# Kernel optimization log

Measured on AMD Instinct MI355X. Metric: run time of the kernel, lower is better.

## Reference

```python
import jax, jax.numpy as jnp
import numpy as np

DIM = 256
CTX_DIM = 256
HEADS = 32
DIM_HEAD = 32
INNER = HEADS * DIM_HEAD


def mish(x):
    return x * jnp.tanh(jax.nn.softplus(x))


def setup_inputs() -> dict:
    key = jax.random.key(0)
    ks = jax.random.split(key, 16)
    B, Lq, Lp = 16, 128, 512
    s = 0.02
    return {
        "x": jax.random.normal(ks[0], (B * Lq, DIM), jnp.float32),
        "context": jax.random.normal(ks[1], (B * Lp, CTX_DIM), jnp.float32),
        "batch_dis": jax.random.normal(ks[2], (B, Lp, Lq, 3), jnp.float32),
        "batch_dis_emb": jax.random.normal(ks[3], (B, Lp, Lq, HEADS), jnp.float32),
        "protein_len": Lp,
        "ligand_len": Lq,
        # params ([in, out] layout, torch Linear transposed)
        "W_qk": jax.random.normal(ks[4], (DIM, INNER), jnp.float32) * s,
        "W_v": jax.random.normal(ks[5], (DIM, INNER), jnp.float32) * s,
        "W_cqk": jax.random.normal(ks[6], (CTX_DIM, INNER), jnp.float32) * s,
        "W_cv": jax.random.normal(ks[7], (CTX_DIM, INNER), jnp.float32) * s,
        "W_m1": jax.random.normal(ks[8], (2 * HEADS, 4 * HEADS), jnp.float32) * s,
        "W_m2": jax.random.normal(ks[9], (4 * HEADS, 2 * HEADS), jnp.float32) * s,
        "b_m2": jnp.zeros((2 * HEADS,), jnp.float32),
        "W_o": jax.random.normal(ks[10], (INNER, DIM), jnp.float32) * s,
        "b_o": jnp.zeros((DIM,), jnp.float32),
        "W_d1": jax.random.normal(ks[11], (HEADS, 2 * HEADS), jnp.float32) * s,
        "b_d1": jnp.zeros((2 * HEADS,), jnp.float32),
        "W_d2": jax.random.normal(ks[12], (2 * HEADS, HEADS), jnp.float32) * s,
        "b_d2": jnp.zeros((HEADS,), jnp.float32),
    }


def reference(x, context, batch_dis, batch_dis_emb, protein_len, ligand_len,
              W_qk, W_v, W_cqk, W_cv, W_m1, W_m2, b_m2, W_o, b_o,
              W_d1, b_d1, W_d2, b_d2):
    h, dh = HEADS, DIM_HEAD
    scale = dh ** -0.5
    B = x.shape[0] // ligand_len
    # projections; split heads: [B, L, h, dh]
    qk = (x @ W_qk).reshape(B, ligand_len, h, dh)
    cqk = (context @ W_cqk).reshape(B, protein_len, h, dh)
    cv = (context @ W_cv).reshape(B, protein_len, h, dh)
    # ligand->protein attention scores: [B, h, Lq, Lp]
    sim = jnp.einsum('bihd,bjhd->bhij', qk, cqk) * scale
    # distance-embedding channels: [B, Lp, Lq, h] -> [B, h, Lq, Lp]
    dis = jnp.transpose(batch_dis_emb, (0, 3, 2, 1))
    s = jnp.concatenate([sim, dis], axis=1)           # [B, 2h, Lq, Lp]
    s = jnp.moveaxis(s, 1, -1)                        # [B, Lq, Lp, 2h]
    s = mish(s @ W_m1) @ W_m2 + b_m2                  # attn_mlp over channel dim
    attn = jax.nn.softmax(s, axis=2)                  # softmax over protein (j)
    # first h heads attend into context values
    out = jnp.einsum('bijh,bjhd->bihd', attn[..., :h], cv)
    out = out.reshape(B * ligand_len, h * dh) @ W_o + b_o   # [N_lig, dim]
    # last h heads aggregate 3D distance vectors
    out_dis = jnp.einsum('bijh,bjid->bidh', attn[..., h:], batch_dis)
    out_dis = out_dis.reshape(B * ligand_len, 3, h)
    out_dis = mish(out_dis @ W_d1 + b_d1) @ W_d2 + b_d2      # [N_lig, 3, h]
    return out, out_dis
```

## Files before the change

kernel.cpp:

```cpp
#include <hip/hip_runtime.h>

typedef unsigned short u16;
typedef unsigned int   u32;
typedef __attribute__((ext_vector_type(8))) short bf16x8;
typedef __attribute__((ext_vector_type(4))) float f32x4;

#define MFMA_BF16 __builtin_amdgcn_mfma_f32_16x16x32_bf16
#define LOG2E 1.4426950408889634f

__device__ __forceinline__ u16 f2bf(float f) {
    u32 x = __builtin_bit_cast(u32, f);
    u32 r = (x + 0x7fffu + ((x >> 16) & 1u)) >> 16;
    return (u16)r;
}
__device__ __forceinline__ u32 cvt_pk_bf16(float lo, float hi) {
    u32 r;
    asm("v_cvt_pk_bf16_f32 %0, %1, %2" : "=v"(r) : "v"(lo), "v"(hi));
    return r;
}
__device__ __forceinline__ float exp2_asm(float x) {
    float r;
    asm("v_exp_f32 %0, %1" : "=v"(r) : "v"(x));
    return r;
}
__device__ __forceinline__ float rcp_asm(float x) {
    float r;
    asm("v_rcp_f32 %0, %1" : "=v"(r) : "v"(x));
    return r;
}
__device__ __forceinline__ float mishf(float x) {
    float e = exp2_asm(x * LOG2E);
    float p = 1.f + e;
    float d = __builtin_fmaf(p, p, 1.f);
    float r = __builtin_fmaf(-2.f, rcp_asm(d), 1.f);
    return x * r;
}

__global__ __launch_bounds__(256) void gemm_mfma(
    const float* __restrict__ A, const float* __restrict__ W, u16* __restrict__ C,
    int M, int N, int K, float scale)
{
    __shared__ u16 As[128 * 40];
    __shared__ u16 Bf[8 * 64 * 8];

    const int tid = threadIdx.x;
    const int lane = tid & 63, wv = tid >> 6;
    const int qd = lane >> 4, ln = lane & 15;
    const int m0 = blockIdx.y * 128, n0 = blockIdx.x * 128;

    f32x4 acc[2][8];
#pragma unroll
    for (int a = 0; a < 2; ++a)
#pragma unroll
        for (int nt = 0; nt < 8; ++nt) acc[a][nt] = (f32x4){0.f, 0.f, 0.f, 0.f};

    for (int k0 = 0; k0 < K; k0 += 32) {
        {
            int r = tid >> 1, kh = (tid & 1) * 16;
            const float* ap = A + (size_t)(m0 + r) * K + k0 + kh;
            float4 a0 = ((const float4*)ap)[0];
            float4 a1 = ((const float4*)ap)[1];
            float4 a2 = ((const float4*)ap)[2];
            float4 a3 = ((const float4*)ap)[3];
            uint4 p0, p1;
            p0.x = cvt_pk_bf16(a0.x, a0.y);
            p0.y = cvt_pk_bf16(a0.z, a0.w);
            p0.z = cvt_pk_bf16(a1.x, a1.y);
            p0.w = cvt_pk_bf16(a1.z, a1.w);
            p1.x = cvt_pk_bf16(a2.x, a2.y);
            p1.y = cvt_pk_bf16(a2.z, a2.w);
            p1.z = cvt_pk_bf16(a3.x, a3.y);
            p1.w = cvt_pk_bf16(a3.z, a3.w);
            *(uint4*)&As[r * 40 + kh]     = p0;
            *(uint4*)&As[r * 40 + kh + 8] = p1;
        }
        {
            int ntA = tid >> 6, q = (tid >> 4) & 3, nn = tid & 15;
#pragma unroll
            for (int h = 0; h < 2; ++h) {
                int nt = ntA + h * 4;
                const float* wp = W + (size_t)(k0 + q * 8) * N + n0 + nt * 16 + nn;
                float w0 = wp[0], w1 = wp[(size_t)1 * N], w2 = wp[(size_t)2 * N], w3 = wp[(size_t)3 * N];
                float w4 = wp[(size_t)4 * N], w5 = wp[(size_t)5 * N], w6 = wp[(size_t)6 * N], w7 = wp[(size_t)7 * N];
                uint4 u;
                u.x = cvt_pk_bf16(w0, w1);
                u.y = cvt_pk_bf16(w2, w3);
                u.z = cvt_pk_bf16(w4, w5);
                u.w = cvt_pk_bf16(w6, w7);
                *(uint4*)&Bf[(nt * 64 + q * 16 + nn) * 8] = u;
            }
        }
        __syncthreads();
        bf16x8 af0 = *(const bf16x8*)&As[(wv * 32 + ln) * 40 + qd * 8];
        bf16x8 af1 = *(const bf16x8*)&As[(wv * 32 + 16 + ln) * 40 + qd * 8];
#pragma unroll
        for (int nt = 0; nt < 8; ++nt) {
            bf16x8 bfr = *(const bf16x8*)&Bf[(nt * 64 + lane) * 8];
            acc[0][nt] = MFMA_BF16(af0, bfr, acc[0][nt], 0, 0, 0);
            acc[1][nt] = MFMA_BF16(af1, bfr, acc[1][nt], 0, 0, 0);
        }
        __syncthreads();
    }
#pragma unroll
    for (int a = 0; a < 2; ++a)
#pragma unroll
        for (int nt = 0; nt < 8; ++nt) {
            u32 pk0 = cvt_pk_bf16(acc[a][nt][0] * scale, acc[a][nt][1] * scale);
            u32 pk1 = cvt_pk_bf16(acc[a][nt][2] * scale, acc[a][nt][3] * scale);
            size_t base = (size_t)(m0 + wv * 32 + a * 16 + qd * 4) * N + n0 + nt * 16 + ln;
            C[base]               = (u16)pk0;
            C[base + (size_t)N]   = (u16)(pk0 >> 16);
            C[base + (size_t)2*N] = (u16)pk1;
            C[base + (size_t)3*N] = (u16)(pk1 >> 16);
        }
}

__global__ __launch_bounds__(256) void transpose_cv(
    const u16* __restrict__ cv, u16* __restrict__ cvT)
{
    __shared__ u16 T[64 * 80];
    const int tid = threadIdx.x;
    const int ct = blockIdx.x * 64, jt = blockIdx.y * 64, b = blockIdx.z;
    {
        int j_l = tid >> 2, seg = tid & 3;
        const u16* src = cv + (size_t)(b * 512 + jt + j_l) * 1024 + ct + seg * 16;
        uint4 v0 = ((const uint4*)src)[0];
        uint4 v1 = ((const uint4*)src)[1];
        u16* tp = &T[seg * 16 * 80 + j_l];
        tp[0*80] = (u16)(v0.x & 0xffff); tp[1*80] = (u16)(v0.x >> 16);
        tp[2*80] = (u16)(v0.y & 0xffff); tp[3*80] = (u16)(v0.y >> 16);
        tp[4*80] = (u16)(v0.z & 0xffff); tp[5*80] = (u16)(v0.z >> 16);
        tp[6*80] = (u16)(v0.w & 0xffff); tp[7*80] = (u16)(v0.w >> 16);
        tp[8*80] = (u16)(v1.x & 0xffff); tp[9*80] = (u16)(v1.x >> 16);
        tp[10*80] = (u16)(v1.y & 0xffff); tp[11*80] = (u16)(v1.y >> 16);
        tp[12*80] = (u16)(v1.z & 0xffff); tp[13*80] = (u16)(v1.z >> 16);
        tp[14*80] = (u16)(v1.w & 0xffff); tp[15*80] = (u16)(v1.w >> 16);
    }
    __syncthreads();
    {
        int ch_l = tid >> 2, sg = tid & 3;
        u16* dst = cvT + (size_t)(b * 1024 + ct + ch_l) * 512 + jt + sg * 16;
        ((uint4*)dst)[0] = *(const uint4*)&T[ch_l * 80 + sg * 16];
        ((uint4*)dst)[1] = *(const uint4*)&T[ch_l * 80 + sg * 16 + 8];
    }
}

__global__ __launch_bounds__(256) void prep(
    const float* __restrict__ Wo, const float* __restrict__ W1, const float* __restrict__ W2,
    u16* __restrict__ WoT, u16* __restrict__ w1b, u16* __restrict__ w2b)
{
    const int bb = blockIdx.x, t = threadIdx.x;
    if (bb < 256) {
#pragma unroll
        for (int kk = 0; kk < 4; ++kk)
            WoT[(size_t)t * 1024 + bb * 4 + kk] = f2bf(Wo[(size_t)(bb * 4 + kk) * 256 + t]);
    } else {
        for (int u = 0; u < 32; ++u) {
            int idx = t + 256 * u;
            int j = idx & 7, lane = (idx >> 3) & 63, f = idx >> 9;
            int n = lane & 15, q = lane >> 4, ntc = f & 7, ks = f >> 3;
            w1b[idx] = f2bf(W1[(ks * 32 + q * 8 + j) * 128 + ntc * 16 + n]);
        }
        for (int u = 0; u < 32; ++u) {
            int idx = t + 256 * u;
            int j = idx & 7, lane = (idx >> 3) & 63, f = idx >> 9;
            int n = lane & 15, q = lane >> 4, ot = f & 3, ks = f >> 2;
            int k = q * 8 + j;
            int ch = ((k & 1) << 4) | (k >> 1);
            w2b[idx] = f2bf(W2[(ks * 32 + ch) * 64 + ot * 16 + n] * LOG2E);
        }
    }
}

__global__ __launch_bounds__(256, 1) void attn5(
    const u16* __restrict__ qk,
    const u16* __restrict__ cqk,
    const u16* __restrict__ cvT,
    const float* __restrict__ bde,
    const float* __restrict__ bdis,
    const u16* __restrict__ w1b, const u16* __restrict__ w2b,
    const float* __restrict__ b2,
    float* __restrict__ partial)
{
    __shared__ __align__(16) char smem[76288];
    u16*   ES  = (u16*)smem;
    u16*   MT  = (u16*)(smem + 20480);
    float* BD  = (float*)(smem + 30720);
    u16*   EST = (u16*)(smem + 34816);
    u16*   W1B = (u16*)(smem + 59904);

    const int tid = threadIdx.x;
    const int lane = tid & 63, wv = tid >> 6;
    const int qd = lane >> 4, ln = lane & 15;
    const int nblk = blockIdx.x;
    const int xcd = nblk & 7, g = nblk >> 3;
    const int b = xcd * 2 + (g & 1);
    const int r2 = g >> 1;
    const int it = r2 >> 2, jq = r2 & 3;
    const int i0 = it * 16;
    const int pidx = (b * 8 + it) * 4 + jq;

    for (int k = tid; k < 4096; k += 256) ((u32*)W1B)[k] = ((const u32*)w1b)[k];

    float b2r[4];
#pragma unroll
    for (int ot = 0; ot < 4; ++ot) b2r[ot] = b2[ot * 16 + ln] * LOG2E;

    bf16x8 qkf[8];
#pragma unroll
    for (int hh = 0; hh < 8; ++hh) {
        int h = wv * 8 + hh;
        qkf[hh] = *(const bf16x8*)(qk + ((size_t)(b * 128 + i0 + ln)) * 1024 + h * 32 + qd * 8);
    }

    const int ii = tid & 15, jj = tid >> 4;

    bf16x8 cqk_pf[8];
    float4 bde_pf[8];
    float bdp0, bdp1, bdp2;
    {
        const u16* crow = cqk + (size_t)(b * 512 + jq * 128 + ln) * 1024 + qd * 8;
#pragma unroll
        for (int hh = 0; hh < 8; ++hh)
            cqk_pf[hh] = *(const bf16x8*)(crow + (wv * 8 + hh) * 32);
#pragma unroll
        for (int s2 = 0; s2 < 4; ++s2) {
            const float* dps = bde + (((size_t)(b * 512 + jq * 128 + ln)) * 128 + i0 + wv * 4 + s2) * 32 + qd * 8;
            bde_pf[s2 * 2]     = ((const float4*)dps)[0];
            bde_pf[s2 * 2 + 1] = ((const float4*)dps)[1];
        }
        const float* sp = bdis + ((size_t)(b * 512 + jq * 128 + jj) * 128 + i0 + ii) * 3;
        bdp0 = sp[0]; bdp1 = sp[1]; bdp2 = sp[2];
        float* dp2 = &BD[(ii * 16 + jj) * 4];
        dp2[0] = bdp0; dp2[1] = bdp1; dp2[2] = bdp2;
    }

    f32x4 oacc[8][2];
#pragma unroll
    for (int a = 0; a < 8; ++a)
#pragma unroll
        for (int c = 0; c < 2; ++c) oacc[a][c] = (f32x4){0.f, 0.f, 0.f, 0.f};
    float dn[4][4] = {};
    float dd[4][3][2] = {};

    __syncthreads();

#pragma clang loop unroll(disable)
    for (int ps = 0; ps < 8; ++ps) {
        const int jg0 = jq * 128 + ps * 16;

        {
            bf16x8 cqk_use[8];
#pragma unroll
            for (int hh = 0; hh < 8; ++hh) cqk_use[hh] = cqk_pf[hh];
#pragma unroll
            for (int hh = 0; hh < 4; ++hh) {
                const int h0 = wv * 8 + hh * 2;
                f32x4 c0 = (f32x4){0.f, 0.f, 0.f, 0.f}, c1 = c0;
                c0 = MFMA_BF16(qkf[hh * 2],     cqk_use[hh * 2],     c0, 0, 0, 0);
                c1 = MFMA_BF16(qkf[hh * 2 + 1], cqk_use[hh * 2 + 1], c1, 0, 0, 0);
#pragma unroll
                for (int r = 0; r < 4; ++r)
                    *(u32*)&ES[((qd * 4 + r) * 16 + ln) * 40 + h0] = cvt_pk_bf16(c0[r], c1[r]);
            }
        }
        __syncthreads();

        const int psn = (ps < 7) ? ps + 1 : 7;
        const int jgn = jq * 128 + psn * 16;
        float4 bde_use[8];
#pragma unroll
        for (int k = 0; k < 8; ++k) bde_use[k] = bde_pf[k];
        {
            const u16* crow = cqk + (size_t)(b * 512 + jgn + ln) * 1024 + qd * 8;
#pragma unroll
            for (int hh = 0; hh < 8; ++hh)
                cqk_pf[hh] = *(const bf16x8*)(crow + (wv * 8 + hh) * 32);
#pragma unroll
            for (int s2 = 0; s2 < 4; ++s2) {
                const float* dps = bde + (((size_t)(b * 512 + jgn + ln)) * 128 + i0 + wv * 4 + s2) * 32 + qd * 8;
                bde_pf[s2 * 2]     = ((const float4*)dps)[0];
                bde_pf[s2 * 2 + 1] = ((const float4*)dps)[1];
            }
            const float* sp = bdis + ((size_t)(b * 512 + jgn + jj) * 128 + i0 + ii) * 3;
            bdp0 = sp[0]; bdp1 = sp[1]; bdp2 = sp[2];
        }

#pragma unroll
        for (int s = 0; s < 4; ++s) {
            const int i_loc = wv * 4 + s;
            bf16x8 af0 = *(const bf16x8*)&ES[(i_loc * 16 + ln) * 40 + qd * 8];
            bf16x8 af1;
            {
                float4 a0 = bde_use[s * 2];
                float4 a1 = bde_use[s * 2 + 1];
                uint4 u;
                u.x = cvt_pk_bf16(a0.x, a0.y);
                u.y = cvt_pk_bf16(a0.z, a0.w);
                u.z = cvt_pk_bf16(a1.x, a1.y);
                u.w = cvt_pk_bf16(a1.z, a1.w);
                af1 = __builtin_bit_cast(bf16x8, u);
            }
            f32x4 uacc[4];
#pragma unroll
            for (int ot = 0; ot < 4; ++ot) uacc[ot] = (f32x4){0.f, 0.f, 0.f, 0.f};
#pragma unroll
            for (int cg = 0; cg < 4; ++cg) {
                u16* mtp = MT + wv * 1280 + (cg & 1) * 640;
                bf16x8 w00 = *(const bf16x8*)&W1B[((cg * 2 + 0) * 64 + lane) * 8];
                bf16x8 w01 = *(const bf16x8*)&W1B[((cg * 2 + 1) * 64 + lane) * 8];
                bf16x8 w10 = *(const bf16x8*)&W1B[((8 + cg * 2 + 0) * 64 + lane) * 8];
                bf16x8 w11 = *(const bf16x8*)&W1B[((8 + cg * 2 + 1) * 64 + lane) * 8];
                f32x4 t0 = (f32x4){0.f, 0.f, 0.f, 0.f}, t1 = t0;
                t0 = MFMA_BF16(af0, w00, t0, 0, 0, 0);
                t0 = MFMA_BF16(af1, w10, t0, 0, 0, 0);
                t1 = MFMA_BF16(af0, w01, t1, 0, 0, 0);
                t1 = MFMA_BF16(af1, w11, t1, 0, 0, 0);
#pragma unroll
                for (int r = 0; r < 4; ++r) {
                    u32 pk = cvt_pk_bf16(mishf(t0[r]), mishf(t1[r]));
                    *(u32*)&mtp[(qd * 4 + r) * 40 + (ln << 1)] = pk;
                }
                bf16x8 ta = *(const bf16x8*)&mtp[ln * 40 + qd * 8];
#pragma unroll
                for (int ot = 0; ot < 4; ++ot) {
                    bf16x8 wf = *(const bf16x8*)(w2b + ((size_t)(cg * 4 + ot) * 64 + lane) * 8);
                    uacc[ot] = MFMA_BF16(ta, wf, uacc[ot], 0, 0, 0);
                }
            }
            float Ev[4][4];
#pragma unroll
            for (int ot = 0; ot < 4; ++ot) {
#pragma unroll
                for (int r = 0; r < 4; ++r) Ev[ot][r] = exp2_asm(uacc[ot][r] + b2r[ot]);
                dn[s][ot] += (Ev[ot][0] + Ev[ot][1]) + (Ev[ot][2] + Ev[ot][3]);
            }
#pragma unroll
            for (int r = 0; r < 4; ++r) {
                float4 bp = *(const float4*)&BD[(i_loc * 16 + qd * 4 + r) * 4];
                dd[s][0][0] += Ev[2][r] * bp.x; dd[s][0][1] += Ev[3][r] * bp.x;
                dd[s][1][0] += Ev[2][r] * bp.y; dd[s][1][1] += Ev[3][r] * bp.y;
                dd[s][2][0] += Ev[2][r] * bp.z; dd[s][2][1] += Ev[3][r] * bp.z;
            }
#pragma unroll
            for (int ot = 0; ot < 2; ++ot) {
                const int base = (ot * 16 + ln) * 392 + i_loc * 24 + qd * 4;
                *(u32*)&EST[base]     = cvt_pk_bf16(Ev[ot][0], Ev[ot][1]);
                *(u32*)&EST[base + 2] = cvt_pk_bf16(Ev[ot][2], Ev[ot][3]);
            }
        }
        __syncthreads();

        {
            float* dp2 = &BD[(ii * 16 + jj) * 4];
            dp2[0] = bdp0; dp2[1] = bdp1; dp2[2] = bdp2;
        }
#pragma unroll
        for (int hh = 0; hh < 8; ++hh) {
            const int h = wv * 8 + hh;
            bf16x8 af = (bf16x8){0, 0, 0, 0, 0, 0, 0, 0};
            if (qd < 2) af = *(const bf16x8*)&EST[h * 392 + ln * 24 + qd * 8];
#pragma unroll
            for (int nt = 0; nt < 2; ++nt) {
                bf16x8 bfr = (bf16x8){0, 0, 0, 0, 0, 0, 0, 0};
                if (qd < 2)
                    bfr = *(const bf16x8*)(cvT + ((size_t)(b * 1024 + h * 32 + nt * 16 + ln)) * 512 + jg0 + qd * 8);
                oacc[hh][nt] = MFMA_BF16(af, bfr, oacc[hh][nt], 0, 0, 0);
            }
        }
    }

    float* P = partial + (size_t)pidx * 18944;
#pragma unroll
    for (int hh = 0; hh < 8; ++hh)
#pragma unroll
        for (int nt = 0; nt < 2; ++nt)
#pragma unroll
            for (int r = 0; r < 4; ++r)
                P[(size_t)(qd * 4 + r) * 1024 + (wv * 8 + hh) * 32 + nt * 16 + ln] = oacc[hh][nt][r];
#pragma unroll
    for (int s = 0; s < 4; ++s)
#pragma unroll
        for (int ot = 0; ot < 4; ++ot) {
            float v = dn[s][ot];
            v += __shfl_xor(v, 16, 64);
            v += __shfl_xor(v, 32, 64);
            if (qd == 0) P[16384 + (wv * 4 + s) * 64 + ot * 16 + ln] = v;
        }
#pragma unroll
    for (int s = 0; s < 4; ++s)
#pragma unroll
        for (int d = 0; d < 3; ++d)
#pragma unroll
            for (int o = 0; o < 2; ++o) {
                float v = dd[s][d][o];
                v += __shfl_xor(v, 16, 64);
                v += __shfl_xor(v, 32, 64);
                if (qd == 0) P[17408 + (wv * 4 + s) * 96 + d * 32 + o * 16 + ln] = v;
            }
}

__global__ __launch_bounds__(256, 2) void finalize(
    const float* __restrict__ partial, const u16* __restrict__ WoT,
    const float* __restrict__ bo,
    const float* __restrict__ Wd1, const float* __restrict__ bd1,
    const float* __restrict__ Wd2, const float* __restrict__ bd2,
    float* __restrict__ out0, float* __restrict__ out1)
{
    __shared__ float denomL[1024];
    __shared__ u16 preL[16 * 1032];
    __shared__ float odisL[1536];
    __shared__ float r1L[3072];

    const int tid = threadIdx.x;
    const int f = blockIdx.x;
    const int b = f >> 3, it = f & 7;
    const int row0 = b * 128 + it * 16;
    const float* P0 = partial + (size_t)(f * 4 + 0) * 18944;
    const float* P1 = partial + (size_t)(f * 4 + 1) * 18944;
    const float* P2 = partial + (size_t)(f * 4 + 2) * 18944;
    const float* P3 = partial + (size_t)(f * 4 + 3) * 18944;

    for (int k = tid; k < 1024; k += 256)
        denomL[k] = P0[16384 + k] + P1[16384 + k] + P2[16384 + k] + P3[16384 + k];
    __syncthreads();

    {
        const int h = tid >> 3;
#pragma unroll
        for (int i = 0; i < 16; ++i) {
            float4 a = *(const float4*)&P0[(size_t)i * 1024 + tid * 4];
            float4 bq = *(const float4*)&P1[(size_t)i * 1024 + tid * 4];
            float4 c = *(const float4*)&P2[(size_t)i * 1024 + tid * 4];
            float4 d = *(const float4*)&P3[(size_t)i * 1024 + tid * 4];
            float rdn = 1.f / denomL[i * 64 + h];
            u32 p0 = cvt_pk_bf16((a.x + bq.x + c.x + d.x) * rdn, (a.y + bq.y + c.y + d.y) * rdn);
            u32 p1 = cvt_pk_bf16((a.z + bq.z + c.z + d.z) * rdn, (a.w + bq.w + c.w + d.w) * rdn);
            *(uint2*)(void*)&preL[i * 1032 + tid * 4] = make_uint2(p0, p1);
        }
    }
    for (int idx = tid; idx < 1536; idx += 256) {
        int i = idx / 96, rm = idx % 96, h = rm & 31;
        odisL[idx] = (P0[17408 + idx] + P1[17408 + idx] + P2[17408 + idx] + P3[17408 + idx])
                     / denomL[i * 64 + 32 + h];
    }
    __syncthreads();

    {
        const int lane = tid & 63, wv = tid >> 6;
        const int qd = lane >> 4, ln = lane & 15;
        f32x4 acc[4];
#pragma unroll
        for (int nt = 0; nt < 4; ++nt) acc[nt] = (f32x4){0.f, 0.f, 0.f, 0.f};
#pragma clang loop unroll(disable)
        for (int ks = 0; ks < 32; ++ks) {
            bf16x8 af = *(const bf16x8*)&preL[ln * 1032 + ks * 32 + qd * 8];
#pragma unroll
            for (int nt = 0; nt < 4; ++nt) {
                bf16x8 wf = *(const bf16x8*)(WoT + ((size_t)(wv * 64 + nt * 16 + ln)) * 1024 + ks * 32 + qd * 8);
                acc[nt] = MFMA_BF16(af, wf, acc[nt], 0, 0, 0);
            }
        }
#pragma unroll
        for (int nt = 0; nt < 4; ++nt) {
            int col = wv * 64 + nt * 16 + ln;
            float bv = bo[col];
#pragma unroll
            for (int r = 0; r < 4; ++r)
                out0[(size_t)(row0 + qd * 4 + r) * 256 + col] = acc[nt][r] + bv;
        }
    }

    for (int idx = tid; idx < 3072; idx += 256) {
        int i = idx / 192, rm = idx % 192, d = rm / 64, c = rm & 63;
        float t = bd1[c];
#pragma unroll
        for (int hh = 0; hh < 32; ++hh)
            t += odisL[i * 96 + d * 32 + hh] * Wd1[hh * 64 + c];
        r1L[idx] = mishf(t);
    }
    __syncthreads();
    for (int idx = tid; idx < 1536; idx += 256) {
        int i = idx / 96, rm = idx % 96, d = rm >> 5, h = rm & 31;
        float v = bd2[h];
#pragma unroll
        for (int c = 0; c < 64; ++c)
            v += r1L[i * 192 + d * 64 + c] * Wd2[c * 32 + h];
        out1[(size_t)(row0 + i) * 96 + d * 32 + h] = v;
    }
}

extern "C" void kernel_launch(void* const* d_in, const int* in_sizes, int n_in,
                              void* d_out, int out_size, void* d_ws, size_t ws_size,
                              hipStream_t stream) {
    const float* x    = (const float*)d_in[0];
    const float* ctx  = (const float*)d_in[1];
    const float* bdis = (const float*)d_in[2];
    const float* bde  = (const float*)d_in[3];
    const float* Wqk  = (const float*)d_in[6];
    const float* Wcqk = (const float*)d_in[8];
    const float* Wcv  = (const float*)d_in[9];
    const float* Wm1  = (const float*)d_in[10];
    const float* Wm2  = (const float*)d_in[11];
    const float* bm2  = (const float*)d_in[12];
    const float* Wo   = (const float*)d_in[13];
    const float* bo   = (const float*)d_in[14];
    const float* Wd1  = (const float*)d_in[15];
    const float* bd1  = (const float*)d_in[16];
    const float* Wd2  = (const float*)d_in[17];
    const float* bd2  = (const float*)d_in[18];

    char* ws = (char*)d_ws;
    u16* qk_ws  = (u16*)(ws);
    u16* cqk_ws = (u16*)(ws + 4194304);
    u16* cvT_ws = (u16*)(ws + 20971520);
    u16* w1b    = (u16*)(ws + 37748736);
    u16* w2b    = (u16*)(ws + 37765120);
    u16* WoT    = (u16*)(ws + 37781504);
    float* part = (float*)(ws + 38305792);
    u16* cv_rm  = (u16*)(ws + 38305792);

    float* out0 = (float*)d_out;
    float* out1 = out0 + (size_t)2048 * 256;

    const float SCALE = 0.17677669529663687f;

    prep<<<257, 256, 0, stream>>>(Wo, Wm1, Wm2, WoT, w1b, w2b);
    gemm_mfma<<<dim3(8, 16), 256, 0, stream>>>(x,   Wqk,  qk_ws,  2048, 1024, 256, SCALE);
    gemm_mfma<<<dim3(8, 64), 256, 0, stream>>>(ctx, Wcqk, cqk_ws, 8192, 1024, 256, 1.0f);
    gemm_mfma<<<dim3(8, 64), 256, 0, stream>>>(ctx, Wcv,  cv_rm,  8192, 1024, 256, 1.0f);
    transpose_cv<<<dim3(16, 8, 16), 256, 0, stream>>>(cv_rm, cvT_ws);
    attn5<<<512, 256, 0, stream>>>(qk_ws, cqk_ws, cvT_ws, bde, bdis, w1b, w2b, bm2, part);
    finalize<<<128, 256, 0, stream>>>(part, WoT, bo, Wd1, bd1, Wd2, bd2, out0, out1);
}
```

Before: 537.5 us.

## Fuse prep, projection GEMMs and cv transpose into one launch

Merges the weight-prep kernel, the three projection GEMMs and the cv transpose into a single kernel whose block index selects the role. The cv GEMM now writes its tile transposed through shared memory directly into cvT, which removes the row-major cv round trip and the separate transpose pass. This cuts four kernel launches and the extra global traffic, at the cost of a larger grid with mixed block roles and two extra shared-memory staging steps in the cv epilogue.

```diff
diff --git a/kernel.cpp b/kernel.cpp
--- a/kernel.cpp
+++ b/kernel.cpp
@@ -36,17 +36,56 @@
     return x * r;
 }
 
-__global__ __launch_bounds__(256) void gemm_mfma(
-    const float* __restrict__ A, const float* __restrict__ W, u16* __restrict__ C,
-    int M, int N, int K, float scale)
+__global__ __launch_bounds__(256) void proj_fused(
+    const float* __restrict__ x,   const float* __restrict__ Wqk,  u16* __restrict__ qk_ws,
+    const float* __restrict__ ctx, const float* __restrict__ Wcqk, u16* __restrict__ cqk_ws,
+    const float* __restrict__ Wcv, u16* __restrict__ cvT,
+    const float* __restrict__ Wo,  const float* __restrict__ W1,   const float* __restrict__ W2,
+    u16* __restrict__ WoT, u16* __restrict__ w1b, u16* __restrict__ w2b,
+    float scale)
 {
-    __shared__ u16 As[128 * 40];
-    __shared__ u16 Bf[8 * 64 * 8];
-
+    __shared__ __align__(16) char smem[18432];
+    const int id = blockIdx.x;
     const int tid = threadIdx.x;
+
+    if (id >= 1152) {
+        const int bb = id - 1152, t = tid;
+        if (bb < 256) {
+#pragma unroll
+            for (int kk = 0; kk < 4; ++kk)
+                WoT[(size_t)t * 1024 + bb * 4 + kk] = f2bf(Wo[(size_t)(bb * 4 + kk) * 256 + t]);
+        } else {
+            for (int u = 0; u < 32; ++u) {
+                int idx = t + 256 * u;
+                int j = idx & 7, lane = (idx >> 3) & 63, f = idx >> 9;
+                int n = lane & 15, q = lane >> 4, ntc = f & 7, ks = f >> 3;
+                w1b[idx] = f2bf(W1[(ks * 32 + q * 8 + j) * 128 + ntc * 16 + n]);
+            }
+            for (int u = 0; u < 32; ++u) {
+                int idx = t + 256 * u;
+                int j = idx & 7, lane = (idx >> 3) & 63, f = idx >> 9;
+                int n = lane & 15, q = lane >> 4, ot = f & 3, ks = f >> 2;
+                int k = q * 8 + j;
+                int ch = ((k & 1) << 4) | (k >> 1);
+                w2b[idx] = f2bf(W2[(ks * 32 + ch) * 64 + ot * 16 + n] * LOG2E);
+            }
+        }
+        return;
+    }
+
+    u16* As = (u16*)smem;
+    u16* Bf = (u16*)(smem + 10240);
+
+    const float* A; const float* W; u16* C = qk_ws;
+    int bx, by; bool cv = false; float sc = 1.0f;
+    if (id < 128)      { A = x;   W = Wqk;  C = qk_ws;  bx = id & 7; by = id >> 3; sc = scale; }
+    else if (id < 640) { A = ctx; W = Wcqk; C = cqk_ws; int i2 = id - 128; bx = i2 & 7; by = i2 >> 3; }
+    else               { A = ctx; W = Wcv;              int i2 = id - 640; bx = i2 & 7; by = i2 >> 3; cv = true; }
+
+    const int K = 256, N = 1024;
     const int lane = tid & 63, wv = tid >> 6;
     const int qd = lane >> 4, ln = lane & 15;
-    const int m0 = blockIdx.y * 128, n0 = blockIdx.x * 128;
+    const int m0 = by * 128, n0 = bx * 128;
 
     f32x4 acc[2][8];
 #pragma unroll
@@ -101,73 +140,48 @@
         }
         __syncthreads();
     }
-#pragma unroll
-    for (int a = 0; a < 2; ++a)
-#pragma unroll
-        for (int nt = 0; nt < 8; ++nt) {
-            u32 pk0 = cvt_pk_bf16(acc[a][nt][0] * scale, acc[a][nt][1] * scale);
-            u32 pk1 = cvt_pk_bf16(acc[a][nt][2] * scale, acc[a][nt][3] * scale);
-            size_t base = (size_t)(m0 + wv * 32 + a * 16 + qd * 4) * N + n0 + nt * 16 + ln;
-            C[base]               = (u16)pk0;
-            C[base + (size_t)N]   = (u16)(pk0 >> 16);
-            C[base + (size_t)2*N] = (u16)pk1;
-            C[base + (size_t)3*N] = (u16)(pk1 >> 16);
-        }
-}
-
-__global__ __launch_bounds__(256) void transpose_cv(
-    const u16* __restrict__ cv, u16* __restrict__ cvT)
-{
-    __shared__ u16 T[64 * 80];
-    const int tid = threadIdx.x;
-    const int ct = blockIdx.x * 64, jt = blockIdx.y * 64, b = blockIdx.z;
-    {
-        int j_l = tid >> 2, seg = tid & 3;
-        const u16* src = cv + (size_t)(b * 512 + jt + j_l) * 1024 + ct + seg * 16;
-        uint4 v0 = ((const uint4*)src)[0];
-        uint4 v1 = ((const uint4*)src)[1];
-        u16* tp = &T[seg * 16 * 80 + j_l];
-        tp[0*80] = (u16)(v0.x & 0xffff); tp[1*80] = (u16)(v0.x >> 16);
-        tp[2*80] = (u16)(v0.y & 0xffff); tp[3*80] = (u16)(v0.y >> 16);
-        tp[4*80] = (u16)(v0.z & 0xffff); tp[5*80] = (u16)(v0.z >> 16);
-        tp[6*80] = (u16)(v0.w & 0xffff); tp[7*80] = (u16)(v0.w >> 16);
-        tp[8*80] = (u16)(v1.x & 0xffff); tp[9*80] = (u16)(v1.x >> 16);
-        tp[10*80] = (u16)(v1.y & 0xffff); tp[11*80] = (u16)(v1.y >> 16);
-        tp[12*80] = (u16)(v1.z & 0xffff); tp[13*80] = (u16)(v1.z >> 16);
-        tp[14*80] = (u16)(v1.w & 0xffff); tp[15*80] = (u16)(v1.w >> 16);
-    }
-    __syncthreads();
-    {
-        int ch_l = tid >> 2, sg = tid & 3;
-        u16* dst = cvT + (size_t)(b * 1024 + ct + ch_l) * 512 + jt + sg * 16;
-        ((uint4*)dst)[0] = *(const uint4*)&T[ch_l * 80 + sg * 16];
-        ((uint4*)dst)[1] = *(const uint4*)&T[ch_l * 80 + sg * 16 + 8];
-    }
-}
-
-__global__ __launch_bounds__(256) void prep(
-    const float* __restrict__ Wo, const float* __restrict__ W1, const float* __restrict__ W2,
-    u16* __restrict__ WoT, u16* __restrict__ w1b, u16* __restrict__ w2b)
-{
-    const int bb = blockIdx.x, t = threadIdx.x;
-    if (bb < 256) {
-#pragma unroll
-        for (int kk = 0; kk < 4; ++kk)
-            WoT[(size_t)t * 1024 + bb * 4 + kk] = f2bf(Wo[(size_t)(bb * 4 + kk) * 256 + t]);
+
+    if (!cv) {
+#pragma unroll
+        for (int a = 0; a < 2; ++a)
+#pragma unroll
+            for (int nt = 0; nt < 8; ++nt) {
+                u32 pk0 = cvt_pk_bf16(acc[a][nt][0] * sc, acc[a][nt][1] * sc);
+                u32 pk1 = cvt_pk_bf16(acc[a][nt][2] * sc, acc[a][nt][3] * sc);
+                size_t base = (size_t)(m0 + wv * 32 + a * 16 + qd * 4) * N + n0 + nt * 16 + ln;
+                C[base]               = (u16)pk0;
+                C[base + (size_t)N]   = (u16)(pk0 >> 16);
+                C[base + (size_t)2*N] = (u16)pk1;
+                C[base + (size_t)3*N] = (u16)(pk1 >> 16);
+            }
     } else {
-        for (int u = 0; u < 32; ++u) {
-            int idx = t + 256 * u;
-            int j = idx & 7, lane = (idx >> 3) & 63, f = idx >> 9;
-            int n = lane & 15, q = lane >> 4, ntc = f & 7, ks = f >> 3;
-            w1b[idx] = f2bf(W1[(ks * 32 + q * 8 + j) * 128 + ntc * 16 + n]);
-        }
-        for (int u = 0; u < 32; ++u) {
-            int idx = t + 256 * u;
-            int j = idx & 7, lane = (idx >> 3) & 63, f = idx >> 9;
-            int n = lane & 15, q = lane >> 4, ot = f & 3, ks = f >> 2;
-            int k = q * 8 + j;
-            int ch = ((k & 1) << 4) | (k >> 1);
-            w2b[idx] = f2bf(W2[(ks * 32 + ch) * 64 + ot * 16 + n] * LOG2E);
+        const int b = m0 >> 9, jt = m0 & 511;
+        u16* T = (u16*)smem;
+#pragma unroll
+        for (int h = 0; h < 2; ++h) {
+            if (h) __syncthreads();
+#pragma unroll
+            for (int a = 0; a < 2; ++a)
+#pragma unroll
+                for (int t2 = 0; t2 < 4; ++t2) {
+                    int nt = h * 4 + t2;
+                    int chl = t2 * 16 + ln;
+                    int row = wv * 32 + a * 16 + qd * 4;
+                    uint2 pk;
+                    pk.x = cvt_pk_bf16(acc[a][nt][0], acc[a][nt][1]);
+                    pk.y = cvt_pk_bf16(acc[a][nt][2], acc[a][nt][3]);
+                    *(uint2*)&T[chl * 136 + row] = pk;
+                }
+            __syncthreads();
+            {
+                int chl = tid >> 2, jseg = (tid & 3) * 32;
+                const uint4* src = (const uint4*)&T[chl * 136 + jseg];
+                u16* dst = cvT + ((size_t)(b * 1024 + n0 + h * 64 + chl)) * 512 + jt + jseg;
+                ((uint4*)dst)[0] = src[0];
+                ((uint4*)dst)[1] = src[1];
+                ((uint4*)dst)[2] = src[2];
+                ((uint4*)dst)[3] = src[3];
+            }
         }
     }
 }
@@ -518,18 +532,15 @@
     u16* w2b    = (u16*)(ws + 37765120);
     u16* WoT    = (u16*)(ws + 37781504);
     float* part = (float*)(ws + 38305792);
-    u16* cv_rm  = (u16*)(ws + 38305792);
 
     float* out0 = (float*)d_out;
     float* out1 = out0 + (size_t)2048 * 256;
 
     const float SCALE = 0.17677669529663687f;
 
-    prep<<<257, 256, 0, stream>>>(Wo, Wm1, Wm2, WoT, w1b, w2b);
-    gemm_mfma<<<dim3(8, 16), 256, 0, stream>>>(x,   Wqk,  qk_ws,  2048, 1024, 256, SCALE);
-    gemm_mfma<<<dim3(8, 64), 256, 0, stream>>>(ctx, Wcqk, cqk_ws, 8192, 1024, 256, 1.0f);
-    gemm_mfma<<<dim3(8, 64), 256, 0, stream>>>(ctx, Wcv,  cv_rm,  8192, 1024, 256, 1.0f);
-    transpose_cv<<<dim3(16, 8, 16), 256, 0, stream>>>(cv_rm, cvT_ws);
+    proj_fused<<<1409, 256, 0, stream>>>(x, Wqk, qk_ws, ctx, Wcqk, cqk_ws,
+                                         Wcv, cvT_ws, Wo, Wm1, Wm2,
+                                         WoT, w1b, w2b, SCALE);
     attn5<<<512, 256, 0, stream>>>(qk_ws, cqk_ws, cvT_ws, bde, bdis, w1b, w2b, bm2, part);
     finalize<<<128, 256, 0, stream>>>(part, WoT, bo, Wd1, bd1, Wd2, bd2, out0, out1);
 }
```

Measured after the change: 506.4 us. 5.8% less time.
